# Performance work log

Hardware: AMD Instinct MI355X
Metric: run time of the kernel (lower is better)

The kernel has to match this reference:

```python
import jax, jax.numpy as jnp
import numpy as np

N_NODES = 100000
N_EDGES = 1600000
DROPOUT_P = 0.5


def setup_inputs() -> dict:
    key = jax.random.key(0)
    k1, k2, k3, k4 = jax.random.split(key, 4)
    x = jax.random.normal(k1, (N_NODES, 128), dtype=jnp.float32)
    edge_index = jax.random.randint(k2, (2, N_EDGES), 0, N_NODES, dtype=jnp.int64)
    W1 = jax.random.normal(k3, (128, 64), dtype=jnp.float32) * (1.0 / np.sqrt(128))
    b1 = jnp.zeros((64,), dtype=jnp.float32)
    W2 = jax.random.normal(k4, (64, 40), dtype=jnp.float32) * (1.0 / np.sqrt(64))
    b2 = jnp.zeros((40,), dtype=jnp.float32)
    return {"x": x, "edge_index": edge_index, "W1": W1, "b1": b1, "W2": W2, "b2": b2}


def reference(x, edge_index, W1, b1, W2, b2):
    n = x.shape[0]
    src, dst = edge_index[0], edge_index[1]
    # GCN symmetric normalization with self-loops: deg = A.sum + 1
    deg = jax.ops.segment_sum(jnp.ones(src.shape[0], x.dtype), dst, num_segments=n) + 1.0
    inv_sqrt = jax.lax.rsqrt(deg)  # [N]
    edge_norm = (inv_sqrt[src] * inv_sqrt[dst])[:, None]  # [E,1]
    self_norm = (inv_sqrt * inv_sqrt)[:, None]            # [N,1]

    def propagate(h):
        # gather source features, scale, scatter-add to destinations; add self-loop term
        agg = jax.ops.segment_sum(h[src] * edge_norm, dst, num_segments=n)
        return agg + h * self_norm

    # layer 1: linear -> aggregate -> bias -> relu -> dropout
    h = propagate(x @ W1) + b1
    h = jax.nn.relu(h)
    keep = 1.0 - DROPOUT_P
    mask = jax.random.bernoulli(jax.random.key(42), keep, h.shape)
    h = jnp.where(mask, h / keep, 0.0)
    # layer 2
    out = propagate(h @ W2) + b2
    return out
```

## Files before the change

### kernel.cpp

```cpp
#include <hip/hip_runtime.h>

#define NN 100000
#define NE 1600000
#define FI 128
#define FH 64
#define FO 40
#define NR 500
#define RSZ 200
#define NBK 512

typedef _Float16 f16;

__device__ __forceinline__ unsigned rotl32(unsigned v, unsigned r) {
    return (v << r) | (v >> (32u - r));
}

__device__ __forceinline__ void threefry_0_42(unsigned x0, unsigned x1,
                                              unsigned& o0, unsigned& o1) {
    const unsigned k0 = 0u, k1 = 42u;
    const unsigned k2 = 0x1BD11BDAu ^ k0 ^ k1;
    x0 += k0; x1 += k1;
#define TFR(r) { x0 += x1; x1 = rotl32(x1, r); x1 ^= x0; }
    TFR(13) TFR(15) TFR(26) TFR(6)   x0 += k1; x1 += k2 + 1u;
    TFR(17) TFR(29) TFR(16) TFR(24)  x0 += k2; x1 += k0 + 2u;
    TFR(13) TFR(15) TFR(26) TFR(6)   x0 += k0; x1 += k1 + 3u;
    TFR(17) TFR(29) TFR(16) TFR(24)  x0 += k1; x1 += k2 + 4u;
    TFR(13) TFR(15) TFR(26) TFR(6)   x0 += k2; x1 += k0 + 5u;
#undef TFR
    o0 = x0; o1 = x1;
}

__global__ __launch_bounds__(256) void k_p1(const int* __restrict__ ei,
                                            int* __restrict__ blkhist) {
    __shared__ int h[NR];
    int t = threadIdx.x, b = blockIdx.x;
    for (int i = t; i < NR; i += 256) h[i] = 0;
    __syncthreads();
    for (int i = b * 256 + t; i < NE; i += NBK * 256) {
        int d = ei[NE + i];
        atomicAdd(&h[d / RSZ], 1);
    }
    __syncthreads();
    for (int i = t; i < NR; i += 256) blkhist[(size_t)b * NR + i] = h[i];
}

__global__ __launch_bounds__(512) void k_scanR1(int* __restrict__ blkhist,
                                                int* __restrict__ rtot) {
    __shared__ int sh[NBK];
    int r = blockIdx.x, t = threadIdx.x;
    int v = blkhist[(size_t)t * NR + r];
    sh[t] = v;
    __syncthreads();
    for (int off = 1; off < NBK; off <<= 1) {
        int u = (t >= off) ? sh[t - off] : 0;
        __syncthreads();
        sh[t] += u;
        __syncthreads();
    }
    blkhist[(size_t)t * NR + r] = sh[t] - v;
    if (t == NBK - 1) rtot[r] = sh[t];
}

__global__ __launch_bounds__(512) void k_scanR2(const int* __restrict__ rtot,
                                                int* __restrict__ rangeBase) {
    __shared__ int sh[512];
    int t = threadIdx.x;
    int v = (t < NR) ? rtot[t] : 0;
    sh[t] = v;
    __syncthreads();
    for (int off = 1; off < 512; off <<= 1) {
        int u = (t >= off) ? sh[t - off] : 0;
        __syncthreads();
        sh[t] += u;
        __syncthreads();
    }
    if (t < NR) rangeBase[t] = sh[t] - v;
    if (t == NR - 1) rangeBase[NR] = sh[t];
}

__global__ __launch_bounds__(256) void k_p2(const int* __restrict__ ei,
                                            const int* __restrict__ blkhist,
                                            const int* __restrict__ rangeBase,
                                            int2* __restrict__ bucket) {
    __shared__ int cur[NR];
    int t = threadIdx.x, b = blockIdx.x;
    for (int i = t; i < NR; i += 256)
        cur[i] = rangeBase[i] + blkhist[(size_t)b * NR + i];
    __syncthreads();
    for (int i = b * 256 + t; i < NE; i += NBK * 256) {
        int s = ei[i];
        int d = ei[NE + i];
        int pos = atomicAdd(&cur[d / RSZ], 1);
        bucket[pos] = make_int2(s, d);
    }
}

__global__ __launch_bounds__(256) void k_p3(const int2* __restrict__ bucket,
                                            const int* __restrict__ rangeBase,
                                            int2* __restrict__ odpk,
                                            float* __restrict__ inv,
                                            int* __restrict__ csr_s) {
    __shared__ int cnt[RSZ];
    __shared__ int base[RSZ];
    __shared__ int sc[256];
    int r = blockIdx.x, t = threadIdx.x;
    int e0 = rangeBase[r], e1 = rangeBase[r + 1];
    int n0 = r * RSZ;
    if (t < RSZ) cnt[t] = 0;
    __syncthreads();
    for (int i = e0 + t; i < e1; i += 256)
        atomicAdd(&cnt[bucket[i].y - n0], 1);
    __syncthreads();
    int v = (t < RSZ) ? cnt[t] : 0;
    sc[t] = v;
    __syncthreads();
    for (int off = 1; off < 256; off <<= 1) {
        int u = (t >= off) ? sc[t - off] : 0;
        __syncthreads();
        sc[t] += u;
        __syncthreads();
    }
    if (t < RSZ) {
        int o = e0 + sc[t] - v;
        odpk[n0 + t] = make_int2(o, v);
        inv[n0 + t] = rsqrtf((float)v + 1.0f);
        base[t] = o;
    }
    __syncthreads();
    for (int i = e0 + t; i < e1; i += 256) {
        int2 sd = bucket[i];
        int p = atomicAdd(&base[sd.y - n0], 1);
        csr_s[p] = sd.x;
    }
}

#define XS_STRIDE 132
__global__ __launch_bounds__(256) void k_gemm1(const float* __restrict__ x,
                                               const float* __restrict__ W1,
                                               const float* __restrict__ inv,
                                               f16* __restrict__ h0s) {
    __shared__ float xs[64 * XS_STRIDE];
    __shared__ float ws[64 * FH];
    int t = threadIdx.x;
    int row0 = blockIdx.x * 64;
    {
        int r = t >> 5;
        int c4 = (t & 31) * 4;
#pragma unroll
        for (int p = 0; p < 8; ++p) {
            int row = row0 + r + p * 8;
            float4 v = make_float4(0.f, 0.f, 0.f, 0.f);
            if (row < NN) v = *(const float4*)&x[(size_t)row * FI + c4];
            *(float4*)&xs[(r + p * 8) * XS_STRIDE + c4] = v;
        }
    }
    float acc[4][4] = {{0.f}};
    int tx4 = (t & 15) * 4;
    int ty4 = (t >> 4) * 4;
#pragma unroll
    for (int half = 0; half < 2; ++half) {
        __syncthreads();
        {
            const float4* Wv = (const float4*)(W1 + half * 64 * FH);
            float4* wv = (float4*)ws;
            for (int i = t; i < 64 * FH / 4; i += 256) wv[i] = Wv[i];
        }
        __syncthreads();
#pragma unroll 2
        for (int k = 0; k < 64; k += 4) {
            float4 a0 = *(const float4*)&xs[(ty4 + 0) * XS_STRIDE + half * 64 + k];
            float4 a1 = *(const float4*)&xs[(ty4 + 1) * XS_STRIDE + half * 64 + k];
            float4 a2 = *(const float4*)&xs[(ty4 + 2) * XS_STRIDE + half * 64 + k];
            float4 a3 = *(const float4*)&xs[(ty4 + 3) * XS_STRIDE + half * 64 + k];
            float4 b0 = *(const float4*)&ws[(k + 0) * FH + tx4];
            float4 b1 = *(const float4*)&ws[(k + 1) * FH + tx4];
            float4 b2 = *(const float4*)&ws[(k + 2) * FH + tx4];
            float4 b3 = *(const float4*)&ws[(k + 3) * FH + tx4];
#define KK1(AE, BV) \
            acc[0][0] = fmaf(a0.AE, BV.x, acc[0][0]); \
            acc[0][1] = fmaf(a0.AE, BV.y, acc[0][1]); \
            acc[0][2] = fmaf(a0.AE, BV.z, acc[0][2]); \
            acc[0][3] = fmaf(a0.AE, BV.w, acc[0][3]); \
            acc[1][0] = fmaf(a1.AE, BV.x, acc[1][0]); \
            acc[1][1] = fmaf(a1.AE, BV.y, acc[1][1]); \
            acc[1][2] = fmaf(a1.AE, BV.z, acc[1][2]); \
            acc[1][3] = fmaf(a1.AE, BV.w, acc[1][3]); \
            acc[2][0] = fmaf(a2.AE, BV.x, acc[2][0]); \
            acc[2][1] = fmaf(a2.AE, BV.y, acc[2][1]); \
            acc[2][2] = fmaf(a2.AE, BV.z, acc[2][2]); \
            acc[2][3] = fmaf(a2.AE, BV.w, acc[2][3]); \
            acc[3][0] = fmaf(a3.AE, BV.x, acc[3][0]); \
            acc[3][1] = fmaf(a3.AE, BV.y, acc[3][1]); \
            acc[3][2] = fmaf(a3.AE, BV.z, acc[3][2]); \
            acc[3][3] = fmaf(a3.AE, BV.w, acc[3][3]);
            KK1(x, b0) KK1(y, b1) KK1(z, b2) KK1(w, b3)
#undef KK1
        }
    }
#pragma unroll
    for (int i = 0; i < 4; ++i) {
        int row = row0 + ty4 + i;
        if (row < NN) {
            float s = inv[row];
            union { f16 h[4]; uint2 u; } p;
            p.h[0] = (f16)(acc[i][0] * s);
            p.h[1] = (f16)(acc[i][1] * s);
            p.h[2] = (f16)(acc[i][2] * s);
            p.h[3] = (f16)(acc[i][3] * s);
            *(uint2*)&h0s[(size_t)row * FH + tx4] = p.u;
        }
    }
}

__global__ __launch_bounds__(256) void k_agg1(const int2* __restrict__ odpk,
                                              const int* __restrict__ csr_s,
                                              const float* __restrict__ inv,
                                              const f16* __restrict__ h0s,
                                              const float* __restrict__ b1,
                                              float* __restrict__ h1) {
    int lane = threadIdx.x & 63;
    int d = __builtin_amdgcn_readfirstlane((int)(blockIdx.x * 4 + (threadIdx.x >> 6)));
    if (d >= NN) return;
    int2 od = odpk[d];
    int start = od.x, deg = od.y;
    float acc0 = 0.f, acc1 = 0.f;
    int k = 0;
    for (; k + 4 <= deg; k += 4) {
        int s0 = csr_s[start + k + 0];
        int s1 = csr_s[start + k + 1];
        int s2 = csr_s[start + k + 2];
        int s3 = csr_s[start + k + 3];
        float v0 = (float)h0s[(size_t)s0 * FH + lane];
        float v1 = (float)h0s[(size_t)s1 * FH + lane];
        float v2 = (float)h0s[(size_t)s2 * FH + lane];
        float v3 = (float)h0s[(size_t)s3 * FH + lane];
        acc0 += v0 + v2;
        acc1 += v1 + v3;
    }
    for (; k < deg; ++k) {
        int s = csr_s[start + k];
        acc0 += (float)h0s[(size_t)s * FH + lane];
    }
    float invd = inv[d];
    float val = (acc0 + acc1 + (float)h0s[(size_t)d * FH + lane]) * invd + b1[lane];
    val = fmaxf(val, 0.f);
    int i = d * FH + lane;
    unsigned o0, o1;
    threefry_0_42(0u, (unsigned)i, o0, o1);
    unsigned wbits = o0 ^ o1;
    h1[i] = (wbits >> 31) ? 0.f : val * 2.f;
}

#define HS_STRIDE 68
__global__ __launch_bounds__(256) void k_gemm2(const float* __restrict__ h,
                                               const float* __restrict__ W2,
                                               const float* __restrict__ inv,
                                               f16* __restrict__ h2s) {
    __shared__ float hs[64 * HS_STRIDE];
    __shared__ float ws[FH * 64];
    int t = threadIdx.x;
    int row0 = blockIdx.x * 64;
    {
        int r = t >> 4;
        int c4 = (t & 15) * 4;
#pragma unroll
        for (int p = 0; p < 4; ++p) {
            int row = row0 + r + p * 16;
            float4 v = make_float4(0.f, 0.f, 0.f, 0.f);
            if (row < NN) v = *(const float4*)&h[(size_t)row * FH + c4];
            *(float4*)&hs[(r + p * 16) * HS_STRIDE + c4] = v;
        }
    }
    for (int i = t; i < FH * 64; i += 256) {
        int r = i >> 6, c = i & 63;
        ws[i] = (c < FO) ? W2[r * FO + c] : 0.f;
    }
    __syncthreads();
    float acc[4][4] = {{0.f}};
    int tx4 = (t & 15) * 4;
    int ty4 = (t >> 4) * 4;
#pragma unroll 2
    for (int k = 0; k < FH; k += 4) {
        float4 a0 = *(const float4*)&hs[(ty4 + 0) * HS_STRIDE + k];
        float4 a1 = *(const float4*)&hs[(ty4 + 1) * HS_STRIDE + k];
        float4 a2 = *(const float4*)&hs[(ty4 + 2) * HS_STRIDE + k];
        float4 a3 = *(const float4*)&hs[(ty4 + 3) * HS_STRIDE + k];
        float4 b0 = *(const float4*)&ws[(k + 0) * 64 + tx4];
        float4 b1 = *(const float4*)&ws[(k + 1) * 64 + tx4];
        float4 b2 = *(const float4*)&ws[(k + 2) * 64 + tx4];
        float4 b3 = *(const float4*)&ws[(k + 3) * 64 + tx4];
#define KK2(AE, BV) \
        acc[0][0] = fmaf(a0.AE, BV.x, acc[0][0]); \
        acc[0][1] = fmaf(a0.AE, BV.y, acc[0][1]); \
        acc[0][2] = fmaf(a0.AE, BV.z, acc[0][2]); \
        acc[0][3] = fmaf(a0.AE, BV.w, acc[0][3]); \
        acc[1][0] = fmaf(a1.AE, BV.x, acc[1][0]); \
        acc[1][1] = fmaf(a1.AE, BV.y, acc[1][1]); \
        acc[1][2] = fmaf(a1.AE, BV.z, acc[1][2]); \
        acc[1][3] = fmaf(a1.AE, BV.w, acc[1][3]); \
        acc[2][0] = fmaf(a2.AE, BV.x, acc[2][0]); \
        acc[2][1] = fmaf(a2.AE, BV.y, acc[2][1]); \
        acc[2][2] = fmaf(a2.AE, BV.z, acc[2][2]); \
        acc[2][3] = fmaf(a2.AE, BV.w, acc[2][3]); \
        acc[3][0] = fmaf(a3.AE, BV.x, acc[3][0]); \
        acc[3][1] = fmaf(a3.AE, BV.y, acc[3][1]); \
        acc[3][2] = fmaf(a3.AE, BV.z, acc[3][2]); \
        acc[3][3] = fmaf(a3.AE, BV.w, acc[3][3]);
        KK2(x, b0) KK2(y, b1) KK2(z, b2) KK2(w, b3)
#undef KK2
    }
#pragma unroll
    for (int i = 0; i < 4; ++i) {
        int row = row0 + ty4 + i;
        if (row < NN) {
            float s = inv[row];
            union { f16 h[4]; uint2 u; } p;
            p.h[0] = (f16)(acc[i][0] * s);
            p.h[1] = (f16)(acc[i][1] * s);
            p.h[2] = (f16)(acc[i][2] * s);
            p.h[3] = (f16)(acc[i][3] * s);
            *(uint2*)&h2s[(size_t)row * FH + tx4] = p.u;
        }
    }
}

__global__ __launch_bounds__(256) void k_agg2(const int2* __restrict__ odpk,
                                              const int* __restrict__ csr_s,
                                              const float* __restrict__ inv,
                                              const f16* __restrict__ h2s,
                                              const float* __restrict__ b2,
                                              float* __restrict__ out) {
    int lane = threadIdx.x & 63;
    int d = __builtin_amdgcn_readfirstlane((int)(blockIdx.x * 4 + (threadIdx.x >> 6)));
    if (d >= NN) return;
    int2 od = odpk[d];
    int start = od.x, deg = od.y;
    float acc0 = 0.f, acc1 = 0.f;
    int k = 0;
    for (; k + 4 <= deg; k += 4) {
        int s0 = csr_s[start + k + 0];
        int s1 = csr_s[start + k + 1];
        int s2 = csr_s[start + k + 2];
        int s3 = csr_s[start + k + 3];
        float v0 = (float)h2s[(size_t)s0 * FH + lane];
        float v1 = (float)h2s[(size_t)s1 * FH + lane];
        float v2 = (float)h2s[(size_t)s2 * FH + lane];
        float v3 = (float)h2s[(size_t)s3 * FH + lane];
        acc0 += v0 + v2;
        acc1 += v1 + v3;
    }
    for (; k < deg; ++k) {
        int s = csr_s[start + k];
        acc0 += (float)h2s[(size_t)s * FH + lane];
    }
    if (lane < FO) {
        float invd = inv[d];
        out[(size_t)d * FO + lane] =
            (acc0 + acc1 + (float)h2s[(size_t)d * FH + lane]) * invd + b2[lane];
    }
}

extern "C" void kernel_launch(void* const* d_in, const int* in_sizes, int n_in,
                              void* d_out, int out_size, void* d_ws, size_t ws_size,
                              hipStream_t stream) {
    const float* x  = (const float*)d_in[0];
    const int*   ei = (const int*)d_in[1];
    const float* W1 = (const float*)d_in[2];
    const float* b1 = (const float*)d_in[3];
    const float* W2 = (const float*)d_in[4];
    const float* b2 = (const float*)d_in[5];
    float* out = (float*)d_out;

    char* ws = (char*)d_ws;
    int*   blkhist   = (int*)ws;
    int*   rtot      = (int*)(ws + (size_t)(1 << 20) + 102400);
    int*   rangeBase = (int*)(ws + (size_t)(1 << 20) + 106496);
    float* inv       = (float*)(ws + (size_t)( 2 << 20));
    int2*  odpk      = (int2*)(ws + (size_t)( 3 << 20));
    int2*  bucket    = (int2*)(ws + (size_t)( 4 << 20));
    f16*   h2s       = (f16*)bucket;
    int*   csr_s     = (int*)(ws + (size_t)(17 << 20));
    f16*   h0s       = (f16*)(ws + (size_t)(24 << 20));
    float* h1        = (float*)(ws + (size_t)(37 << 20));

    k_p1<<<NBK, 256, 0, stream>>>(ei, blkhist);
    k_scanR1<<<NR, 512, 0, stream>>>(blkhist, rtot);
    k_scanR2<<<1, 512, 0, stream>>>(rtot, rangeBase);
    k_p2<<<NBK, 256, 0, stream>>>(ei, blkhist, rangeBase, bucket);
    k_p3<<<NR, 256, 0, stream>>>(bucket, rangeBase, odpk, inv, csr_s);

    int gblk = (NN + 63) / 64;
    k_gemm1<<<gblk, 256, 0, stream>>>(x, W1, inv, h0s);
    k_agg1<<<NN / 4, 256, 0, stream>>>(odpk, csr_s, inv, h0s, b1, h1);

    k_gemm2<<<gblk, 256, 0, stream>>>(h1, W2, inv, h2s);
    k_agg2<<<NN / 4, 256, 0, stream>>>(odpk, csr_s, inv, h2s, b2, out);
}
```

Baseline: 202.6 us.

## Pad CSR neighbor lists to multiples of four and gather four edges per wave

CSR construction pads each node's neighbor list to a multiple of four, filling the gaps with a dummy node whose feature row is zeroed. The aggregation kernels then split each wave into four 16-lane groups, each loading a different neighbor's row as 8-byte vectors, and combine the groups with cross-lane shuffles. The goal is more memory-level parallelism and wider loads in the gather phase. In exchange the kernels do extra padding work, use more workspace (buffers are shifted), and need shuffle reductions plus a ballot-based dropout mask.

```diff
diff --git a/kernel.cpp b/kernel.cpp
--- a/kernel.cpp
+++ b/kernel.cpp
@@ -30,6 +30,19 @@
     o0 = x0; o1 = x1;
 }
 
+__device__ __forceinline__ void unpack2(unsigned u, float& lo, float& hi) {
+    union { unsigned u; f16 h[2]; } c;
+    c.u = u;
+    lo = (float)c.h[0];
+    hi = (float)c.h[1];
+}
+
+__device__ __forceinline__ int sel4(int p, int s0, int s1, int s2, int s3) {
+    int t0 = (p & 1) ? s1 : s0;
+    int t1 = (p & 1) ? s3 : s2;
+    return (p & 2) ? t1 : t0;
+}
+
 __global__ __launch_bounds__(256) void k_p1(const int* __restrict__ ei,
                                             int* __restrict__ blkhist) {
     __shared__ int h[NR];
@@ -105,14 +118,19 @@
     __shared__ int sc[256];
     int r = blockIdx.x, t = threadIdx.x;
     int e0 = rangeBase[r], e1 = rangeBase[r + 1];
+    int padBase = e0 + 3 * RSZ * r;
     int n0 = r * RSZ;
     if (t < RSZ) cnt[t] = 0;
     __syncthreads();
     for (int i = e0 + t; i < e1; i += 256)
         atomicAdd(&cnt[bucket[i].y - n0], 1);
     __syncthreads();
-    int v = (t < RSZ) ? cnt[t] : 0;
-    sc[t] = v;
+    int v = 0, vp = 0;
+    if (t < RSZ) {
+        v = cnt[t];
+        vp = (v + 3) & ~3;
+    }
+    sc[t] = vp;
     __syncthreads();
     for (int off = 1; off < 256; off <<= 1) {
         int u = (t >= off) ? sc[t - off] : 0;
@@ -120,9 +138,10 @@
         sc[t] += u;
         __syncthreads();
     }
+    int o = 0;
     if (t < RSZ) {
-        int o = e0 + sc[t] - v;
-        odpk[n0 + t] = make_int2(o, v);
+        o = padBase + sc[t] - vp;
+        odpk[n0 + t] = make_int2(o, vp);
         inv[n0 + t] = rsqrtf((float)v + 1.0f);
         base[t] = o;
     }
@@ -131,6 +150,10 @@
         int2 sd = bucket[i];
         int p = atomicAdd(&base[sd.y - n0], 1);
         csr_s[p] = sd.x;
+    }
+    __syncthreads();
+    if (t < RSZ) {
+        for (int j = v; j < vp; ++j) csr_s[o + j] = NN;
     }
 }
 
@@ -208,6 +231,8 @@
             p.h[2] = (f16)(acc[i][2] * s);
             p.h[3] = (f16)(acc[i][3] * s);
             *(uint2*)&h0s[(size_t)row * FH + tx4] = p.u;
+        } else if (row == NN) {
+            *(uint2*)&h0s[(size_t)row * FH + tx4] = make_uint2(0u, 0u);
         }
     }
 }
@@ -221,34 +246,63 @@
     int lane = threadIdx.x & 63;
     int d = __builtin_amdgcn_readfirstlane((int)(blockIdx.x * 4 + (threadIdx.x >> 6)));
     if (d >= NN) return;
+    int p = lane >> 4;
+    int c4 = (lane & 15) * 4;
+    size_t q8 = (size_t)(lane & 15) * 8;
+    const char* hb = (const char*)h0s;
     int2 od = odpk[d];
-    int start = od.x, deg = od.y;
-    float acc0 = 0.f, acc1 = 0.f;
+    int start = od.x, degp = od.y;
+    float a0 = 0.f, a1 = 0.f, a2 = 0.f, a3 = 0.f;
     int k = 0;
-    for (; k + 4 <= deg; k += 4) {
-        int s0 = csr_s[start + k + 0];
-        int s1 = csr_s[start + k + 1];
-        int s2 = csr_s[start + k + 2];
-        int s3 = csr_s[start + k + 3];
-        float v0 = (float)h0s[(size_t)s0 * FH + lane];
-        float v1 = (float)h0s[(size_t)s1 * FH + lane];
-        float v2 = (float)h0s[(size_t)s2 * FH + lane];
-        float v3 = (float)h0s[(size_t)s3 * FH + lane];
-        acc0 += v0 + v2;
-        acc1 += v1 + v3;
-    }
-    for (; k < deg; ++k) {
-        int s = csr_s[start + k];
-        acc0 += (float)h0s[(size_t)s * FH + lane];
-    }
+    for (; k + 8 <= degp; k += 8) {
+        int s0 = csr_s[start + k + 0], s1 = csr_s[start + k + 1];
+        int s2 = csr_s[start + k + 2], s3 = csr_s[start + k + 3];
+        int s4 = csr_s[start + k + 4], s5 = csr_s[start + k + 5];
+        int s6 = csr_s[start + k + 6], s7 = csr_s[start + k + 7];
+        int ia = sel4(p, s0, s1, s2, s3);
+        int ib = sel4(p, s4, s5, s6, s7);
+        uint2 ua = *(const uint2*)(hb + ((size_t)ia << 7) + q8);
+        uint2 ub = *(const uint2*)(hb + ((size_t)ib << 7) + q8);
+        float f0, f1, f2, f3;
+        unpack2(ua.x, f0, f1); unpack2(ua.y, f2, f3);
+        a0 += f0; a1 += f1; a2 += f2; a3 += f3;
+        unpack2(ub.x, f0, f1); unpack2(ub.y, f2, f3);
+        a0 += f0; a1 += f1; a2 += f2; a3 += f3;
+    }
+    if (k < degp) {
+        int s0 = csr_s[start + k + 0], s1 = csr_s[start + k + 1];
+        int s2 = csr_s[start + k + 2], s3 = csr_s[start + k + 3];
+        int ia = sel4(p, s0, s1, s2, s3);
+        uint2 ua = *(const uint2*)(hb + ((size_t)ia << 7) + q8);
+        float f0, f1, f2, f3;
+        unpack2(ua.x, f0, f1); unpack2(ua.y, f2, f3);
+        a0 += f0; a1 += f1; a2 += f2; a3 += f3;
+    }
+    a0 += __shfl_xor(a0, 16, 64); a0 += __shfl_xor(a0, 32, 64);
+    a1 += __shfl_xor(a1, 16, 64); a1 += __shfl_xor(a1, 32, 64);
+    a2 += __shfl_xor(a2, 16, 64); a2 += __shfl_xor(a2, 32, 64);
+    a3 += __shfl_xor(a3, 16, 64); a3 += __shfl_xor(a3, 32, 64);
     float invd = inv[d];
-    float val = (acc0 + acc1 + (float)h0s[(size_t)d * FH + lane]) * invd + b1[lane];
-    val = fmaxf(val, 0.f);
-    int i = d * FH + lane;
+    uint2 su = *(const uint2*)(hb + ((size_t)d << 7) + q8);
+    float s0, s1, s2, s3;
+    unpack2(su.x, s0, s1); unpack2(su.y, s2, s3);
+    float4 bv = *(const float4*)&b1[c4];
+    float v0 = fmaxf((a0 + s0) * invd + bv.x, 0.f);
+    float v1 = fmaxf((a1 + s1) * invd + bv.y, 0.f);
+    float v2 = fmaxf((a2 + s2) * invd + bv.z, 0.f);
+    float v3 = fmaxf((a3 + s3) * invd + bv.w, 0.f);
     unsigned o0, o1;
-    threefry_0_42(0u, (unsigned)i, o0, o1);
-    unsigned wbits = o0 ^ o1;
-    h1[i] = (wbits >> 31) ? 0.f : val * 2.f;
+    threefry_0_42(0u, (unsigned)(d * FH + lane), o0, o1);
+    unsigned long long m = __ballot((int)(((o0 ^ o1) >> 31) ^ 1u));
+    unsigned mm = (unsigned)(m >> c4) & 15u;
+    if (lane < 16) {
+        float4 st;
+        st.x = (mm & 1u) ? v0 * 2.f : 0.f;
+        st.y = (mm & 2u) ? v1 * 2.f : 0.f;
+        st.z = (mm & 4u) ? v2 * 2.f : 0.f;
+        st.w = (mm & 8u) ? v3 * 2.f : 0.f;
+        *(float4*)&h1[(size_t)d * FH + c4] = st;
+    }
 }
 
 #define HS_STRIDE 68
@@ -320,6 +374,8 @@
             p.h[2] = (f16)(acc[i][2] * s);
             p.h[3] = (f16)(acc[i][3] * s);
             *(uint2*)&h2s[(size_t)row * FH + tx4] = p.u;
+        } else if (row == NN) {
+            *(uint2*)&h2s[(size_t)row * FH + tx4] = make_uint2(0u, 0u);
         }
     }
 }
@@ -333,30 +389,54 @@
     int lane = threadIdx.x & 63;
     int d = __builtin_amdgcn_readfirstlane((int)(blockIdx.x * 4 + (threadIdx.x >> 6)));
     if (d >= NN) return;
+    int p = lane >> 4;
+    int c4 = (lane & 15) * 4;
+    size_t q8 = (size_t)(lane & 15) * 8;
+    const char* hb = (const char*)h2s;
     int2 od = odpk[d];
-    int start = od.x, deg = od.y;
-    float acc0 = 0.f, acc1 = 0.f;
+    int start = od.x, degp = od.y;
+    float a0 = 0.f, a1 = 0.f, a2 = 0.f, a3 = 0.f;
     int k = 0;
-    for (; k + 4 <= deg; k += 4) {
-        int s0 = csr_s[start + k + 0];
-        int s1 = csr_s[start + k + 1];
-        int s2 = csr_s[start + k + 2];
-        int s3 = csr_s[start + k + 3];
-        float v0 = (float)h2s[(size_t)s0 * FH + lane];
-        float v1 = (float)h2s[(size_t)s1 * FH + lane];
-        float v2 = (float)h2s[(size_t)s2 * FH + lane];
-        float v3 = (float)h2s[(size_t)s3 * FH + lane];
-        acc0 += v0 + v2;
-        acc1 += v1 + v3;
-    }
-    for (; k < deg; ++k) {
-        int s = csr_s[start + k];
-        acc0 += (float)h2s[(size_t)s * FH + lane];
-    }
-    if (lane < FO) {
+    for (; k + 8 <= degp; k += 8) {
+        int s0 = csr_s[start + k + 0], s1 = csr_s[start + k + 1];
+        int s2 = csr_s[start + k + 2], s3 = csr_s[start + k + 3];
+        int s4 = csr_s[start + k + 4], s5 = csr_s[start + k + 5];
+        int s6 = csr_s[start + k + 6], s7 = csr_s[start + k + 7];
+        int ia = sel4(p, s0, s1, s2, s3);
+        int ib = sel4(p, s4, s5, s6, s7);
+        uint2 ua = *(const uint2*)(hb + ((size_t)ia << 7) + q8);
+        uint2 ub = *(const uint2*)(hb + ((size_t)ib << 7) + q8);
+        float f0, f1, f2, f3;
+        unpack2(ua.x, f0, f1); unpack2(ua.y, f2, f3);
+        a0 += f0; a1 += f1; a2 += f2; a3 += f3;
+        unpack2(ub.x, f0, f1); unpack2(ub.y, f2, f3);
+        a0 += f0; a1 += f1; a2 += f2; a3 += f3;
+    }
+    if (k < degp) {
+        int s0 = csr_s[start + k + 0], s1 = csr_s[start + k + 1];
+        int s2 = csr_s[start + k + 2], s3 = csr_s[start + k + 3];
+        int ia = sel4(p, s0, s1, s2, s3);
+        uint2 ua = *(const uint2*)(hb + ((size_t)ia << 7) + q8);
+        float f0, f1, f2, f3;
+        unpack2(ua.x, f0, f1); unpack2(ua.y, f2, f3);
+        a0 += f0; a1 += f1; a2 += f2; a3 += f3;
+    }
+    a0 += __shfl_xor(a0, 16, 64); a0 += __shfl_xor(a0, 32, 64);
+    a1 += __shfl_xor(a1, 16, 64); a1 += __shfl_xor(a1, 32, 64);
+    a2 += __shfl_xor(a2, 16, 64); a2 += __shfl_xor(a2, 32, 64);
+    a3 += __shfl_xor(a3, 16, 64); a3 += __shfl_xor(a3, 32, 64);
+    if (lane < 10) {
         float invd = inv[d];
-        out[(size_t)d * FO + lane] =
-            (acc0 + acc1 + (float)h2s[(size_t)d * FH + lane]) * invd + b2[lane];
+        uint2 su = *(const uint2*)(hb + ((size_t)d << 7) + q8);
+        float s0, s1, s2, s3;
+        unpack2(su.x, s0, s1); unpack2(su.y, s2, s3);
+        float4 bv = *(const float4*)&b2[c4];
+        float4 st;
+        st.x = (a0 + s0) * invd + bv.x;
+        st.y = (a1 + s1) * invd + bv.y;
+        st.z = (a2 + s2) * invd + bv.z;
+        st.w = (a3 + s3) * invd + bv.w;
+        *(float4*)&out[(size_t)d * FO + c4] = st;
     }
 }
 
@@ -380,8 +460,8 @@
     int2*  bucket    = (int2*)(ws + (size_t)( 4 << 20));
     f16*   h2s       = (f16*)bucket;
     int*   csr_s     = (int*)(ws + (size_t)(17 << 20));
-    f16*   h0s       = (f16*)(ws + (size_t)(24 << 20));
-    float* h1        = (float*)(ws + (size_t)(37 << 20));
+    f16*   h0s       = (f16*)(ws + (size_t)(25 << 20));
+    float* h1        = (float*)(ws + (size_t)(38 << 20));
 
     k_p1<<<NBK, 256, 0, stream>>>(ei, blkhist);
     k_scanR1<<<NR, 512, 0, stream>>>(blkhist, rtot);
```

After: 186.2 us. -8.1%, faster.
